# Optimization experiments

Measured on AMD Instinct MI355X. Metric: run time of the kernel, lower is better.

## Reference

```python
import jax, jax.numpy as jnp
import numpy as np

L, D, H, FF = 4, 256, 8, 1024
B, S = 4, 1024
HD = D // H
EPS = 1e-5


def layer_norm(x, g, b):
    mu = jnp.mean(x, axis=-1, keepdims=True)
    var = jnp.mean(jnp.square(x - mu), axis=-1, keepdims=True)
    return (x - mu) * jax.lax.rsqrt(var + EPS) * g + b


def setup_inputs() -> dict:
    key = jax.random.key(0)
    ks = jax.random.split(key, 16)
    sd = 0.02
    return {
        "x": jax.random.normal(ks[0], (B, S, D), dtype=jnp.float32),
        "mask": jnp.ones((B, S), dtype=jnp.int32),
        # per-layer stacked params (leading dim L); Linear stored as (in, out)
        "qkv_w": jax.random.normal(ks[1], (L, D, 3 * D), dtype=jnp.float32) * sd,
        "qkv_b": jnp.zeros((L, 3 * D), dtype=jnp.float32),
        "fc_w": jax.random.normal(ks[2], (L, D, D), dtype=jnp.float32) * sd,
        "fc_b": jnp.zeros((L, D), dtype=jnp.float32),
        "ln1_g": jnp.ones((L, D), dtype=jnp.float32),
        "ln1_b": jnp.zeros((L, D), dtype=jnp.float32),
        "ln2_g": jnp.ones((L, D), dtype=jnp.float32),
        "ln2_b": jnp.zeros((L, D), dtype=jnp.float32),
        "ff1_w": jax.random.normal(ks[3], (L, D, FF), dtype=jnp.float32) * sd,
        "ff1_b": jnp.zeros((L, FF), dtype=jnp.float32),
        "ff2_w": jax.random.normal(ks[4], (L, FF, D), dtype=jnp.float32) * sd,
        "ff2_b": jnp.zeros((L, D), dtype=jnp.float32),
    }


def reference(x, mask, qkv_w, qkv_b, fc_w, fc_b, ln1_g, ln1_b, ln2_g, ln2_b,
              ff1_w, ff1_b, ff2_w, ff2_b):
    # mask: 1 = valid token, 0 = pad
    neg_inf = jnp.finfo(x.dtype).min
    key_mask = (mask == 0)[:, None, None, :]  # [B,1,1,S]
    for l in range(L):
        residual = x
        qkv = x @ qkv_w[l] + qkv_b[l]                       # [B,S,3D]
        q, k, v = jnp.split(qkv, 3, axis=-1)
        q = q.reshape(B, S, H, HD).transpose(0, 2, 1, 3)    # [B,H,S,hd]
        k = k.reshape(B, S, H, HD).transpose(0, 2, 1, 3)
        v = v.reshape(B, S, H, HD).transpose(0, 2, 1, 3)
        attn = jnp.einsum('bhqd,bhkd->bhqk', q, k)          # scale=1 (scale=False)
        attn = jnp.where(key_mask, neg_inf, attn)
        attn = jax.nn.softmax(attn, axis=-1)
        o = jnp.einsum('bhqk,bhkd->bhqd', attn, v)
        o = o.transpose(0, 2, 1, 3).reshape(B, S, D)
        o = o @ fc_w[l] + fc_b[l]
        x = layer_norm(o + residual, ln1_g[l], ln1_b[l])    # after_norm=True
        residual = x
        h = jax.nn.relu(x @ ff1_w[l] + ff1_b[l])
        h = h @ ff2_w[l] + ff2_b[l]
        x = layer_norm(residual + h, ln2_g[l], ln2_b[l])
    return x
```

## Files before the change

### kernel.cpp

```cpp
#include <hip/hip_runtime.h>
#include <hip/hip_bf16.h>
#include <math.h>

#define NL 4
#define DMODEL 256
#define NH 8
#define FFDIM 1024
#define BB 4
#define SS 1024
#define HDIM 32
#define MROWS (BB * SS)
#define LN_EPS 1e-5f

typedef __bf16 bf16x8 __attribute__((ext_vector_type(8)));
typedef float f32x4 __attribute__((ext_vector_type(4)));
typedef short s16x4 __attribute__((ext_vector_type(4)));
typedef unsigned int u32;

__device__ __forceinline__ ushort f2bf(float f) {
    uint u = __builtin_bit_cast(uint, f);
    u += 0x7fff + ((u >> 16) & 1);
    return (ushort)(u >> 16);
}
__device__ __forceinline__ uint pack2(float a, float b) {
    return (uint)f2bf(a) | ((uint)f2bf(b) << 16);
}

__device__ __forceinline__ int xcd_swz(int bid, int nwg) {
    return (bid & 7) * (nwg >> 3) + (bid >> 3);
}

template<int N> __device__ __forceinline__ void vmcnt_wait() {
    asm volatile("s_waitcnt vmcnt(%0)" :: "n"(N) : "memory");
}
__device__ __forceinline__ void raw_barrier() {
    asm volatile("s_barrier" ::: "memory");
}
__device__ __forceinline__ void lgkm0() {
    asm volatile("s_waitcnt lgkmcnt(0)" ::: "memory");
}

__device__ __forceinline__ void async_ld16(const void* g, void* l) {
    __builtin_amdgcn_global_load_lds(
        (const __attribute__((address_space(1))) u32*)g,
        (__attribute__((address_space(3))) u32*)l, 16, 0, 0);
}

#if __has_builtin(__builtin_amdgcn_ds_read_tr16_b64)
#define TR_BUILTIN 1
#else
#define TR_BUILTIN 0
#endif

__device__ __forceinline__ s16x4 tr16(const ushort* p) {
    __attribute__((address_space(3))) s16x4* ap =
        (__attribute__((address_space(3))) s16x4*)p;
#if TR_BUILTIN
    return __builtin_amdgcn_ds_read_tr16_b64(ap);
#else
    s16x4 r;
    asm volatile("ds_read_b64_tr_b16 %0, %1" : "=v"(r) : "v"(ap) : "memory");
    return r;
#endif
}
__device__ __forceinline__ void tr_fence() {
#if !TR_BUILTIN
    asm volatile("s_waitcnt lgkmcnt(0)" ::: "memory");
    __builtin_amdgcn_sched_barrier(0);
#endif
}

__global__ __launch_bounds__(256)
void wconv_all(const float* __restrict__ qkv_w, const float* __restrict__ fc_w,
               const float* __restrict__ ff1_w, const float* __restrict__ ff2_w,
               ushort* __restrict__ wq, ushort* __restrict__ wfc,
               ushort* __restrict__ wf1, ushort* __restrict__ wf2)
{
    const int l = blockIdx.z;
    int t = blockIdx.x;
    const float* src; ushort* dst; int K, N, nx;
    if (t < 192)      {          src = qkv_w; dst = wq;  K = 256;  N = 768;  nx = 24; }
    else if (t < 256) { t -= 192; src = fc_w;  dst = wfc; K = 256;  N = 256;  nx = 8; }
    else if (t < 512) { t -= 256; src = ff1_w; dst = wf1; K = 256;  N = 1024; nx = 32; }
    else              { t -= 512; src = ff2_w; dst = wf2; K = 1024; N = 256;  nx = 8; }
    src += (size_t)l * K * N;
    dst += (size_t)l * K * N;
    const int n0 = (t % nx) * 32, k0 = (t / nx) * 32;

    __shared__ ushort tt[32][33];
    const int tn = threadIdx.x & 31, tk8 = threadIdx.x >> 5;
    #pragma unroll
    for (int i = 0; i < 4; ++i)
        tt[tn][tk8 + i * 8] = f2bf(src[(size_t)(k0 + tk8 + i * 8) * N + n0 + tn]);
    __syncthreads();
    #pragma unroll
    for (int i = 0; i < 4; ++i)
        dst[(size_t)(n0 + tk8 + i * 8) * K + k0 + tn] = tt[tk8 + i * 8][tn];
}

__global__ __launch_bounds__(256)
void convert_x(const float* __restrict__ xin, float* __restrict__ x,
               ushort* __restrict__ xb)
{
    const size_t i = ((size_t)blockIdx.x * 256 + threadIdx.x) * 4;
    const float4 v = *reinterpret_cast<const float4*>(xin + i);
    *reinterpret_cast<float4*>(x + i) = v;
    uint2 p = make_uint2(pack2(v.x, v.y), pack2(v.z, v.w));
    *reinterpret_cast<uint2*>(xb + i) = p;
}

template<int BM, int BN, int WM, int WN, int ACT, int OBF>
__global__ __launch_bounds__(256)
void gemm_mfma(const ushort* __restrict__ A, const ushort* __restrict__ WT,
               const float* __restrict__ bias, float* __restrict__ Cf,
               ushort* __restrict__ Cb, int N, int K)
{
    constexpr int BK = 64;
    constexpr int WR = BM / WM;
    constexpr int WC = BN / WN;
    constexpr int MR = WR / 16, NR = WC / 16;
    constexpr int LSTG = BM / 32 + BN / 32;
    __shared__ __align__(16) ushort As[2][BM * BK];
    __shared__ __align__(16) ushort Bs[2][BN * BK];

    const int tid = threadIdx.x;
    const int lin = blockIdx.y * gridDim.x + blockIdx.x;
    const int work = xcd_swz(lin, gridDim.x * gridDim.y);
    const int m0 = (work / gridDim.x) * BM, n0 = (work % gridDim.x) * BN;
    const int wid = tid >> 6, lane = tid & 63;
    const int g = lane >> 4, c = lane & 15;
    const int wr = wid / WN, wc = wid % WN;

    auto stage = [&](int buf, int k0) {
        #pragma unroll
        for (int it = 0; it < (BM * BK * 2) / 4096; ++it) {
            const int o = tid * 16 + it * 4096;
            const int r = o >> 7;
            const int cb = (o & 127) ^ ((r & 7) << 4);
            async_ld16(A + (size_t)(m0 + r) * K + k0 + (cb >> 1),
                       (char*)&As[buf][0] + o);
        }
        #pragma unroll
        for (int it = 0; it < (BN * BK * 2) / 4096; ++it) {
            const int o = tid * 16 + it * 4096;
            const int r = o >> 7;
            const int cb = (o & 127) ^ ((r & 7) << 4);
            async_ld16(WT + (size_t)(n0 + r) * K + k0 + (cb >> 1),
                       (char*)&Bs[buf][0] + o);
        }
    };

    f32x4 acc[MR][NR] = {};

    stage(0, 0);

    int cur = 0;
    for (int k0 = 0; k0 < K; k0 += BK, cur ^= 1) {
        if (k0 + BK < K) { stage(cur ^ 1, k0 + BK); vmcnt_wait<LSTG>(); }
        else             { vmcnt_wait<0>(); }
        raw_barrier();

        #pragma unroll
        for (int ks = 0; ks < 2; ++ks) {
            bf16x8 af[MR], bfr[NR];
            #pragma unroll
            for (int mi = 0; mi < MR; ++mi) {
                const int row = wr * WR + mi * 16 + c;
                af[mi] = *(const bf16x8*)((const char*)&As[cur][0]
                    + row * 128 + ((ks * 64 + g * 16) ^ ((row & 7) << 4)));
            }
            #pragma unroll
            for (int ni = 0; ni < NR; ++ni) {
                const int row = wc * WC + ni * 16 + c;
                bfr[ni] = *(const bf16x8*)((const char*)&Bs[cur][0]
                    + row * 128 + ((ks * 64 + g * 16) ^ ((row & 7) << 4)));
            }
            #pragma unroll
            for (int mi = 0; mi < MR; ++mi)
                #pragma unroll
                for (int ni = 0; ni < NR; ++ni)
                    acc[mi][ni] = __builtin_amdgcn_mfma_f32_16x16x32_bf16(
                        af[mi], bfr[ni], acc[mi][ni], 0, 0, 0);
        }
        raw_barrier();
    }

    float bv[NR];
    #pragma unroll
    for (int ni = 0; ni < NR; ++ni)
        bv[ni] = bias[n0 + wc * WC + ni * 16 + c];

    #pragma unroll
    for (int mi = 0; mi < MR; ++mi) {
        #pragma unroll
        for (int j = 0; j < 4; ++j) {
            const int row = m0 + wr * WR + mi * 16 + g * 4 + j;
            #pragma unroll
            for (int ni = 0; ni < NR; ++ni) {
                float v = acc[mi][ni][j] + bv[ni];
                if (ACT) v = fmaxf(v, 0.f);
                const int col = n0 + wc * WC + ni * 16 + c;
                if (OBF) Cb[(size_t)row * N + col] = f2bf(v);
                else     Cf[(size_t)row * N + col] = v;
            }
        }
    }
}

__global__ __launch_bounds__(512)
void mlp_fused(const ushort* __restrict__ Aattn, const ushort* __restrict__ Wfc,
               const float* __restrict__ bfc, const float* __restrict__ g1,
               const float* __restrict__ be1, const ushort* __restrict__ W1,
               const float* __restrict__ b1, const ushort* __restrict__ W2,
               const float* __restrict__ b2, const float* __restrict__ g2,
               const float* __restrict__ be2, float* __restrict__ x,
               ushort* __restrict__ xb)
{
    __shared__ __align__(16) ushort As3[3][16 * 64];
    __shared__ __align__(16) ushort Bs3[3][256 * 64];
    __shared__ __align__(16) ushort ybf[16 * 256];
    __shared__ __align__(16) ushort hbuf[16 * 1024];
    __shared__ float rsum[4][16], rsq[4][16], mval[16], ival[16];

    const int tid = threadIdx.x;
    const int m0 = blockIdx.x * 16;
    const int wid = tid >> 6, lane = tid & 63;
    const int g = lane >> 4, c = lane & 15;
    const bool consumer = (tid < 256);
    const int ptid = tid - 256;
    const int at = tid - 384;

    auto stage_step = [&](int s, int b) {
        const ushort* bsrc; int ldk;
        if (s < 4)       { bsrc = Wfc + s * 64; ldk = 256; }
        else if (s < 20) { const int t = s - 4;
                           bsrc = W1 + (size_t)((t >> 2) * 256) * 256 + (t & 3) * 64;
                           ldk = 256; }
        else             { const int t = s - 20; bsrc = W2 + t * 64; ldk = 1024; }
        #pragma unroll
        for (int it = 0; it < 8; ++it) {
            const int o = ptid * 16 + it * 4096;
            const int r = o >> 7;
            const int cb = (o & 127) ^ ((r & 7) << 4);
            async_ld16(bsrc + (size_t)r * ldk + (cb >> 1), (char*)&Bs3[b][0] + o);
        }
        if (s < 4 && at >= 0) {
            const int o = at * 16;
            const int r = o >> 7;
            const int cb = (o & 127) ^ ((r & 7) << 4);
            async_ld16(Aattn + (size_t)(m0 + r) * 256 + s * 64 + (cb >> 1),
                       (char*)&As3[b][0] + o);
        }
    };

    f32x4 acc[4] = {};
    float res[4][4];

    if (!consumer) {
        stage_step(0, 0);
        stage_step(1, 1);
        if (wid >= 6) vmcnt_wait<9>(); else vmcnt_wait<8>();
    }
    raw_barrier();

    #pragma unroll 1
    for (int s = 0; s < 36; ++s) {
        if (s == 4) {
            if (consumer) {
                float bv[4];
                #pragma unroll
                for (int ni = 0; ni < 4; ++ni)
                    bv[ni] = bfc[wid * 64 + ni * 16 + c];
                #pragma unroll
                for (int j = 0; j < 4; ++j) {
                    const int row = g * 4 + j;
                    float sm = 0.f;
                    #pragma unroll
                    for (int ni = 0; ni < 4; ++ni) {
                        const int col = wid * 64 + ni * 16 + c;
                        float vv = acc[ni][j] + bv[ni]
                                 + x[(size_t)(m0 + row) * 256 + col];
                        acc[ni][j] = vv;
                        sm += vv;
                    }
                    #pragma unroll
                    for (int off = 1; off < 16; off <<= 1) sm += __shfl_xor(sm, off);
                    if (c == 0) rsum[wid][row] = sm;
                }
            }
            lgkm0(); raw_barrier();
            if (consumer && tid < 16)
                mval[tid] = (rsum[0][tid] + rsum[1][tid] + rsum[2][tid]
                             + rsum[3][tid]) * (1.f / 256);
            lgkm0(); raw_barrier();
            if (consumer) {
                #pragma unroll
                for (int j = 0; j < 4; ++j) {
                    const int row = g * 4 + j;
                    const float mean = mval[row];
                    float q = 0.f;
                    #pragma unroll
                    for (int ni = 0; ni < 4; ++ni) {
                        const float d = acc[ni][j] - mean;
                        q += d * d;
                    }
                    #pragma unroll
                    for (int off = 1; off < 16; off <<= 1) q += __shfl_xor(q, off);
                    if (c == 0) rsq[wid][row] = q;
                }
            }
            lgkm0(); raw_barrier();
            if (consumer && tid < 16) {
                const float q = rsq[0][tid] + rsq[1][tid] + rsq[2][tid] + rsq[3][tid];
                ival[tid] = rsqrtf(q * (1.f / 256) + LN_EPS);
            }
            lgkm0(); raw_barrier();
            if (consumer) {
                float gl[4], bl[4];
                #pragma unroll
                for (int ni = 0; ni < 4; ++ni) {
                    const int col = wid * 64 + ni * 16 + c;
                    gl[ni] = g1[col]; bl[ni] = be1[col];
                }
                #pragma unroll
                for (int j = 0; j < 4; ++j) {
                    const int row = g * 4 + j;
                    const float mean = mval[row], inv = ival[row];
                    #pragma unroll
                    for (int ni = 0; ni < 4; ++ni) {
                        const int col = wid * 64 + ni * 16 + c;
                        const float y = (acc[ni][j] - mean) * inv * gl[ni] + bl[ni];
                        res[ni][j] = y;
                        const int byteo = row * 512 + ((col * 2) ^ ((row & 7) << 4));
                        *(ushort*)((char*)ybf + byteo) = f2bf(y);
                        acc[ni][j] = 0.f;
                    }
                }
            }
            lgkm0(); raw_barrier();
        }
        if (s == 20) { lgkm0(); raw_barrier(); }

        if (consumer) {
            const int b = s % 3;
            #pragma unroll
            for (int ks = 0; ks < 2; ++ks) {
                bf16x8 af;
                if (s < 4) {
                    af = *(const bf16x8*)((const char*)&As3[b][0]
                        + c * 128 + ((ks * 64 + g * 16) ^ ((c & 7) << 4)));
                } else if (s < 20) {
                    const int kk = (s - 4) & 3;
                    const int kbyte = (kk * 64 + ks * 32 + g * 8) * 2;
                    af = *(const bf16x8*)((const char*)ybf
                        + c * 512 + (kbyte ^ ((c & 7) << 4)));
                } else {
                    const int t = s - 20;
                    const int kbyte = (t * 64 + ks * 32 + g * 8) * 2;
                    af = *(const bf16x8*)((const char*)hbuf
                        + c * 2048 + (kbyte ^ ((c & 7) << 4)));
                }
                #pragma unroll
                for (int ni = 0; ni < 4; ++ni) {
                    const int row = wid * 64 + ni * 16 + c;
                    const bf16x8 bf = *(const bf16x8*)((const char*)&Bs3[b][0]
                        + row * 128 + ((ks * 64 + g * 16) ^ ((row & 7) << 4)));
                    acc[ni] = __builtin_amdgcn_mfma_f32_16x16x32_bf16(
                        af, bf, acc[ni], 0, 0, 0);
                }
            }
        } else {
            if (s + 2 < 36) {
                stage_step(s + 2, (s + 2) % 3);
                if (s + 2 < 4 && wid >= 6) vmcnt_wait<9>();
                else                       vmcnt_wait<8>();
            } else {
                vmcnt_wait<0>();
            }
        }
        raw_barrier();

        if (consumer && s >= 4 && s < 20 && ((s - 4) & 3) == 3) {
            const int nt = (s - 4) >> 2;
            #pragma unroll
            for (int j = 0; j < 4; ++j) {
                const int row = g * 4 + j;
                #pragma unroll
                for (int ni = 0; ni < 4; ++ni) {
                    const int col = nt * 256 + wid * 64 + ni * 16 + c;
                    const float h = fmaxf(acc[ni][j] + b1[col], 0.f);
                    const int byteo = row * 2048 + ((col * 2) ^ ((row & 7) << 4));
                    *(ushort*)((char*)hbuf + byteo) = f2bf(h);
                    acc[ni][j] = 0.f;
                }
            }
        }
    }

    if (consumer) {
        float bv[4];
        #pragma unroll
        for (int ni = 0; ni < 4; ++ni)
            bv[ni] = b2[wid * 64 + ni * 16 + c];
        #pragma unroll
        for (int j = 0; j < 4; ++j) {
            const int row = g * 4 + j;
            float sm = 0.f;
            #pragma unroll
            for (int ni = 0; ni < 4; ++ni) {
                float vv = acc[ni][j] + bv[ni] + res[ni][j];
                acc[ni][j] = vv;
                sm += vv;
            }
            #pragma unroll
            for (int off = 1; off < 16; off <<= 1) sm += __shfl_xor(sm, off);
            if (c == 0) rsum[wid][row] = sm;
        }
    }
    lgkm0(); raw_barrier();
    if (consumer && tid < 16)
        mval[tid] = (rsum[0][tid] + rsum[1][tid] + rsum[2][tid] + rsum[3][tid])
                    * (1.f / 256);
    lgkm0(); raw_barrier();
    if (consumer) {
        #pragma unroll
        for (int j = 0; j < 4; ++j) {
            const int row = g * 4 + j;
            const float mean = mval[row];
            float q = 0.f;
            #pragma unroll
            for (int ni = 0; ni < 4; ++ni) {
                const float d = acc[ni][j] - mean;
                q += d * d;
            }
            #pragma unroll
            for (int off = 1; off < 16; off <<= 1) q += __shfl_xor(q, off);
            if (c == 0) rsq[wid][row] = q;
        }
    }
    lgkm0(); raw_barrier();
    if (consumer && tid < 16) {
        const float q = rsq[0][tid] + rsq[1][tid] + rsq[2][tid] + rsq[3][tid];
        ival[tid] = rsqrtf(q * (1.f / 256) + LN_EPS);
    }
    lgkm0(); raw_barrier();
    if (consumer) {
        float gl[4], bl[4];
        #pragma unroll
        for (int ni = 0; ni < 4; ++ni) {
            const int col = wid * 64 + ni * 16 + c;
            gl[ni] = g2[col]; bl[ni] = be2[col];
        }
        #pragma unroll
        for (int j = 0; j < 4; ++j) {
            const int row = g * 4 + j;
            const float mean = mval[row], inv = ival[row];
            #pragma unroll
            for (int ni = 0; ni < 4; ++ni) {
                const int col = wid * 64 + ni * 16 + c;
                const float y = (acc[ni][j] - mean) * inv * gl[ni] + bl[ni];
                x[(size_t)(m0 + row) * 256 + col] = y;
                xb[(size_t)(m0 + row) * 256 + col] = f2bf(y);
            }
        }
    }
}

__global__ __launch_bounds__(512)
void attn_mfma8(const ushort* __restrict__ qkv, const int* __restrict__ mask,
                ushort* __restrict__ out)
{
    const int tid = threadIdx.x;
    const int lane = tid & 63, wid = tid >> 6;
    const int g = lane >> 4, c = lane & 15;
    const int work = xcd_swz(blockIdx.x, 256);
    const int qblk = work & 7;
    const int bh = work >> 3;
    const int h = bh & (NH - 1), b = bh >> 3;
    const int q0 = qblk * 128 + wid * 16;

    __shared__ __align__(16) ushort Kb[2][128 * 32];
    __shared__ __align__(16) ushort Vs[2][2][128][16];
    __shared__ __align__(16) ushort Pl[8][16][136];
    __shared__ __align__(16) float  sbias[SS];
    __shared__ int mflag[8];

    const ushort* base  = qkv + (size_t)b * SS * 768;
    const ushort* kbase = base + DMODEL + h * HDIM;
    const ushort* vbase = base + 2 * DMODEL + h * HDIM;

    {
        const int i = tid * 2;
        const int2 mv = *reinterpret_cast<const int2*>(mask + b * SS + i);
        float2 bv;
        bv.x = mv.x ? 0.f : -3.4e38f;
        bv.y = mv.y ? 0.f : -3.4e38f;
        *reinterpret_cast<float2*>(&sbias[i]) = bv;
        const int miss = __any(!(mv.x && mv.y));
        if (lane == 0) mflag[wid] = miss;
    }

    const bf16x8 qfrag = *(const bf16x8*)(
        base + (size_t)(q0 + c) * 768 + h * HDIM + g * 8);

    const int o16   = tid * 16;
    const int krow  = o16 >> 6;
    const int kin   = (o16 & 63) ^ ((krow & 3) << 4);
    const int vhalf = o16 >> 12;
    const int vkey  = (o16 & 4095) >> 5;
    const int vd    = vhalf * 16 + (((o16 >> 4) & 1) << 3);

    #define STAGE(buf, koff)                                                   \
        do {                                                                   \
            async_ld16(kbase + (size_t)((koff) + krow) * 768 + (kin >> 1),     \
                       (char*)&Kb[buf][0] + o16);                              \
            async_ld16(vbase + (size_t)((koff) + vkey) * 768 + vd,             \
                       (char*)&Vs[buf][0][0][0] + o16);                        \
        } while (0)

    STAGE(0, 0);
    lgkm0();
    raw_barrier();
    const int anyMasked = mflag[0] | mflag[1] | mflag[2] | mflag[3]
                        | mflag[4] | mflag[5] | mflag[6] | mflag[7];

    float m = -1e30f, lpart = 0.f;
    f32x4 o0 = {0.f, 0.f, 0.f, 0.f}, o1 = {0.f, 0.f, 0.f, 0.f};
    const f32x4 zf = {0.f, 0.f, 0.f, 0.f};

    for (int t = 0; t < 8; ++t) {
        const int cur = t & 1;
        if (t < 7) { STAGE(cur ^ 1, (t + 1) * 128); vmcnt_wait<2>(); }
        else       { vmcnt_wait<0>(); }
        raw_barrier();

        f32x4 s[8];
        __builtin_amdgcn_s_setprio(1);
        #pragma unroll
        for (int kt = 0; kt < 8; ++kt) {
            const int row = kt * 16 + c;
            const bf16x8 kf = *(const bf16x8*)((const char*)&Kb[cur][0]
                + row * 64 + ((g * 16) ^ ((c & 3) << 4)));
            s[kt] = __builtin_amdgcn_mfma_f32_16x16x32_bf16(kf, qfrag, zf, 0, 0, 0);
        }
        __builtin_amdgcn_s_setprio(0);

        if (anyMasked) {
            #pragma unroll
            for (int kt = 0; kt < 8; ++kt) {
                const f32x4 bv = *reinterpret_cast<const f32x4*>(
                    &sbias[t * 128 + kt * 16 + g * 4]);
                #pragma unroll
                for (int r = 0; r < 4; ++r) s[kt][r] += bv[r];
            }
        }

        union UU { s16x4 h[2]; bf16x8 v; };
        UU u0[4], u1[4];
        #pragma unroll
        for (int ks = 0; ks < 4; ++ks) {
            const int vr0 = ks * 32 + g * 8;
            u0[ks].h[0] = tr16(&Vs[cur][0][vr0][c]);
            u0[ks].h[1] = tr16(&Vs[cur][0][vr0 + 4][c]);
            u1[ks].h[0] = tr16(&Vs[cur][1][vr0][c]);
            u1[ks].h[1] = tr16(&Vs[cur][1][vr0 + 4][c]);
        }

        float mx = fmaxf(fmaxf(s[0][0], s[0][1]), fmaxf(s[0][2], s[0][3]));
        #pragma unroll
        for (int kt = 1; kt < 8; ++kt)
            mx = fmaxf(mx, fmaxf(fmaxf(s[kt][0], s[kt][1]),
                                 fmaxf(s[kt][2], s[kt][3])));
        if (!__all(mx <= m + 8.f)) {
            float fm = fmaxf(mx, __shfl_xor(mx, 16));
            fm = fmaxf(fm, __shfl_xor(fm, 32));
            const float mn = fmaxf(m, fm);
            const float sc = __expf(m - mn);
            m = mn;
            lpart *= sc;
            float scr[4];
            #pragma unroll
            for (int r = 0; r < 4; ++r) scr[r] = __shfl(sc, g * 4 + r);
            #pragma unroll
            for (int r = 0; r < 4; ++r) { o0[r] *= scr[r]; o1[r] *= scr[r]; }
        }

        float ls = 0.f;
        #pragma unroll
        for (int kt = 0; kt < 8; ++kt) {
            const float p0 = __expf(s[kt][0] - m);
            const float p1 = __expf(s[kt][1] - m);
            const float p2 = __expf(s[kt][2] - m);
            const float p3 = __expf(s[kt][3] - m);
            ls += (p0 + p1) + (p2 + p3);
            uint2 pk2 = make_uint2(pack2(p0, p1), pack2(p2, p3));
            *reinterpret_cast<uint2*>(&Pl[wid][c][kt * 16 + g * 4]) = pk2;
        }
        lpart += ls;

        tr_fence();
        __builtin_amdgcn_s_setprio(1);
        #pragma unroll
        for (int ks = 0; ks < 4; ++ks) {
            const bf16x8 pa = *(const bf16x8*)&Pl[wid][c][ks * 32 + g * 8];
            o0 = __builtin_amdgcn_mfma_f32_16x16x32_bf16(pa, u0[ks].v, o0, 0, 0, 0);
            o1 = __builtin_amdgcn_mfma_f32_16x16x32_bf16(pa, u1[ks].v, o1, 0, 0, 0);
        }
        __builtin_amdgcn_s_setprio(0);
        raw_barrier();
    }
    #undef STAGE

    float lsum = lpart;
    lsum += __shfl_xor(lsum, 16);
    lsum += __shfl_xor(lsum, 32);
    const float rs = 1.f / lsum;
    float inv[4];
    #pragma unroll
    for (int r = 0; r < 4; ++r) inv[r] = __shfl(rs, g * 4 + r);
    #pragma unroll
    for (int r = 0; r < 4; ++r) {
        ushort* op = out + (size_t)(b * SS + q0 + g * 4 + r) * DMODEL + h * HDIM;
        op[c]      = f2bf(o0[r] * inv[r]);
        op[16 + c] = f2bf(o1[r] * inv[r]);
    }
}

extern "C" void kernel_launch(void* const* d_in, const int* in_sizes, int n_in,
                              void* d_out, int out_size, void* d_ws, size_t ws_size,
                              hipStream_t stream)
{
    const float* x_in   = (const float*)d_in[0];
    const int*   maskp  = (const int*)d_in[1];
    const float* qkv_w  = (const float*)d_in[2];
    const float* qkv_b  = (const float*)d_in[3];
    const float* fc_w   = (const float*)d_in[4];
    const float* fc_b   = (const float*)d_in[5];
    const float* ln1_g  = (const float*)d_in[6];
    const float* ln1_b  = (const float*)d_in[7];
    const float* ln2_g  = (const float*)d_in[8];
    const float* ln2_b  = (const float*)d_in[9];
    const float* ff1_w  = (const float*)d_in[10];
    const float* ff1_b  = (const float*)d_in[11];
    const float* ff2_w  = (const float*)d_in[12];
    const float* ff2_b  = (const float*)d_in[13];

    float* x = (float*)d_out;

    ushort* wt_qkv = (ushort*)d_ws;
    ushort* wt_fc  = wt_qkv + (size_t)NL * 768 * 256;
    ushort* wt_ff1 = wt_fc  + (size_t)NL * 256 * 256;
    ushort* wt_ff2 = wt_ff1 + (size_t)NL * 1024 * 256;
    ushort* big    = wt_ff2 + (size_t)NL * 256 * 1024;
    ushort* attn_bf= big + (size_t)MROWS * FFDIM;
    ushort* x_bf   = attn_bf + (size_t)MROWS * DMODEL;

    wconv_all<<<dim3(768, 1, NL), 256, 0, stream>>>(
        qkv_w, fc_w, ff1_w, ff2_w, wt_qkv, wt_fc, wt_ff1, wt_ff2);
    convert_x<<<dim3(MROWS * DMODEL / 1024), 256, 0, stream>>>(x_in, x, x_bf);

    for (int l = 0; l < NL; ++l) {
        gemm_mfma<64, 64, 2, 2, 0, 1><<<dim3(12, 64), 256, 0, stream>>>(
            x_bf, wt_qkv + (size_t)l * 768 * 256, qkv_b + l * 768,
            nullptr, big, 768, 256);
        attn_mfma8<<<dim3(256), 512, 0, stream>>>(big, maskp, attn_bf);
        mlp_fused<<<dim3(256), 512, 0, stream>>>(
            attn_bf, wt_fc + (size_t)l * 256 * 256, fc_b + l * 256,
            ln1_g + l * DMODEL, ln1_b + l * DMODEL,
            wt_ff1 + (size_t)l * 1024 * 256, ff1_b + l * FFDIM,
            wt_ff2 + (size_t)l * 256 * 1024, ff2_b + l * DMODEL,
            ln2_g + l * DMODEL, ln2_b + l * DMODEL, x, x_bf);
    }
}
```

Before: 230.2 us.

## Replace producer/consumer warp split in fused MLP with all-warp compute and loads

```diff
diff --git a/kernel.cpp b/kernel.cpp
--- a/kernel.cpp
+++ b/kernel.cpp
@@ -220,17 +220,15 @@
     __shared__ __align__(16) ushort Bs3[3][256 * 64];
     __shared__ __align__(16) ushort ybf[16 * 256];
     __shared__ __align__(16) ushort hbuf[16 * 1024];
-    __shared__ float rsum[4][16], rsq[4][16], mval[16], ival[16];
+    __shared__ float rsum[8][16], rsq[8][16], mval[16], ival[16];
 
     const int tid = threadIdx.x;
     const int m0 = blockIdx.x * 16;
     const int wid = tid >> 6, lane = tid & 63;
     const int g = lane >> 4, c = lane & 15;
-    const bool consumer = (tid < 256);
-    const int ptid = tid - 256;
-    const int at = tid - 384;
-
-    auto stage_step = [&](int s, int b) {
+
+    auto stage_step = [&](int s) {
+        const int b = s % 3;
         const ushort* bsrc; int ldk;
         if (s < 4)       { bsrc = Wfc + s * 64; ldk = 256; }
         else if (s < 20) { const int t = s - 4;
@@ -238,14 +236,14 @@
                            ldk = 256; }
         else             { const int t = s - 20; bsrc = W2 + t * 64; ldk = 1024; }
         #pragma unroll
-        for (int it = 0; it < 8; ++it) {
-            const int o = ptid * 16 + it * 4096;
+        for (int it = 0; it < 4; ++it) {
+            const int o = tid * 16 + it * 8192;
             const int r = o >> 7;
             const int cb = (o & 127) ^ ((r & 7) << 4);
             async_ld16(bsrc + (size_t)r * ldk + (cb >> 1), (char*)&Bs3[b][0] + o);
         }
-        if (s < 4 && at >= 0) {
-            const int o = at * 16;
+        if (s < 4 && tid < 128) {
+            const int o = tid * 16;
             const int r = o >> 7;
             const int cb = (o & 127) ^ ((r & 7) << 4);
             async_ld16(Aattn + (size_t)(m0 + r) * 256 + s * 64 + (cb >> 1),
@@ -253,141 +251,126 @@
         }
     };
 
-    f32x4 acc[4] = {};
-    float res[4][4];
-
-    if (!consumer) {
-        stage_step(0, 0);
-        stage_step(1, 1);
-        if (wid >= 6) vmcnt_wait<9>(); else vmcnt_wait<8>();
-    }
-    raw_barrier();
+    f32x4 acc[2] = {};
+    float res[2][4];
+
+    stage_step(0);
+    stage_step(1);
 
     #pragma unroll 1
     for (int s = 0; s < 36; ++s) {
         if (s == 4) {
-            if (consumer) {
-                float bv[4];
-                #pragma unroll
-                for (int ni = 0; ni < 4; ++ni)
-                    bv[ni] = bfc[wid * 64 + ni * 16 + c];
-                #pragma unroll
-                for (int j = 0; j < 4; ++j) {
-                    const int row = g * 4 + j;
-                    float sm = 0.f;
-                    #pragma unroll
-                    for (int ni = 0; ni < 4; ++ni) {
-                        const int col = wid * 64 + ni * 16 + c;
-                        float vv = acc[ni][j] + bv[ni]
-                                 + x[(size_t)(m0 + row) * 256 + col];
-                        acc[ni][j] = vv;
-                        sm += vv;
-                    }
-                    #pragma unroll
-                    for (int off = 1; off < 16; off <<= 1) sm += __shfl_xor(sm, off);
-                    if (c == 0) rsum[wid][row] = sm;
-                }
-            }
-            lgkm0(); raw_barrier();
-            if (consumer && tid < 16)
-                mval[tid] = (rsum[0][tid] + rsum[1][tid] + rsum[2][tid]
-                             + rsum[3][tid]) * (1.f / 256);
-            lgkm0(); raw_barrier();
-            if (consumer) {
-                #pragma unroll
-                for (int j = 0; j < 4; ++j) {
-                    const int row = g * 4 + j;
-                    const float mean = mval[row];
-                    float q = 0.f;
-                    #pragma unroll
-                    for (int ni = 0; ni < 4; ++ni) {
-                        const float d = acc[ni][j] - mean;
-                        q += d * d;
-                    }
-                    #pragma unroll
-                    for (int off = 1; off < 16; off <<= 1) q += __shfl_xor(q, off);
-                    if (c == 0) rsq[wid][row] = q;
-                }
-            }
-            lgkm0(); raw_barrier();
-            if (consumer && tid < 16) {
-                const float q = rsq[0][tid] + rsq[1][tid] + rsq[2][tid] + rsq[3][tid];
-                ival[tid] = rsqrtf(q * (1.f / 256) + LN_EPS);
-            }
-            lgkm0(); raw_barrier();
-            if (consumer) {
-                float gl[4], bl[4];
-                #pragma unroll
-                for (int ni = 0; ni < 4; ++ni) {
-                    const int col = wid * 64 + ni * 16 + c;
-                    gl[ni] = g1[col]; bl[ni] = be1[col];
-                }
-                #pragma unroll
-                for (int j = 0; j < 4; ++j) {
-                    const int row = g * 4 + j;
-                    const float mean = mval[row], inv = ival[row];
-                    #pragma unroll
-                    for (int ni = 0; ni < 4; ++ni) {
-                        const int col = wid * 64 + ni * 16 + c;
-                        const float y = (acc[ni][j] - mean) * inv * gl[ni] + bl[ni];
-                        res[ni][j] = y;
-                        const int byteo = row * 512 + ((col * 2) ^ ((row & 7) << 4));
-                        *(ushort*)((char*)ybf + byteo) = f2bf(y);
-                        acc[ni][j] = 0.f;
-                    }
-                }
-            }
-            lgkm0(); raw_barrier();
-        }
-        if (s == 20) { lgkm0(); raw_barrier(); }
-
-        if (consumer) {
-            const int b = s % 3;
-            #pragma unroll
-            for (int ks = 0; ks < 2; ++ks) {
-                bf16x8 af;
-                if (s < 4) {
-                    af = *(const bf16x8*)((const char*)&As3[b][0]
-                        + c * 128 + ((ks * 64 + g * 16) ^ ((c & 7) << 4)));
-                } else if (s < 20) {
-                    const int kk = (s - 4) & 3;
-                    const int kbyte = (kk * 64 + ks * 32 + g * 8) * 2;
-                    af = *(const bf16x8*)((const char*)ybf
-                        + c * 512 + (kbyte ^ ((c & 7) << 4)));
-                } else {
-                    const int t = s - 20;
-                    const int kbyte = (t * 64 + ks * 32 + g * 8) * 2;
-                    af = *(const bf16x8*)((const char*)hbuf
-                        + c * 2048 + (kbyte ^ ((c & 7) << 4)));
-                }
-                #pragma unroll
-                for (int ni = 0; ni < 4; ++ni) {
-                    const int row = wid * 64 + ni * 16 + c;
-                    const bf16x8 bf = *(const bf16x8*)((const char*)&Bs3[b][0]
-                        + row * 128 + ((ks * 64 + g * 16) ^ ((row & 7) << 4)));
-                    acc[ni] = __builtin_amdgcn_mfma_f32_16x16x32_bf16(
-                        af, bf, acc[ni], 0, 0, 0);
-                }
-            }
-        } else {
-            if (s + 2 < 36) {
-                stage_step(s + 2, (s + 2) % 3);
-                if (s + 2 < 4 && wid >= 6) vmcnt_wait<9>();
-                else                       vmcnt_wait<8>();
-            } else {
-                vmcnt_wait<0>();
-            }
-        }
-        raw_barrier();
-
-        if (consumer && s >= 4 && s < 20 && ((s - 4) & 3) == 3) {
-            const int nt = (s - 4) >> 2;
+            float bv[2], gl[2], bl[2];
+            #pragma unroll
+            for (int ni = 0; ni < 2; ++ni) {
+                const int col = wid * 32 + ni * 16 + c;
+                bv[ni] = bfc[col]; gl[ni] = g1[col]; bl[ni] = be1[col];
+            }
             #pragma unroll
             for (int j = 0; j < 4; ++j) {
                 const int row = g * 4 + j;
-                #pragma unroll
-                for (int ni = 0; ni < 4; ++ni) {
-                    const int col = nt * 256 + wid * 64 + ni * 16 + c;
+                float sm = 0.f;
+                #pragma unroll
+                for (int ni = 0; ni < 2; ++ni) {
+                    const int col = wid * 32 + ni * 16 + c;
+                    float vv = acc[ni][j] + bv[ni] + x[(size_t)(m0 + row) * 256 + col];
+                    acc[ni][j] = vv;
+                    sm += vv;
+                }
+                #pragma unroll
+                for (int off = 1; off < 16; off <<= 1) sm += __shfl_xor(sm, off);
+                if (c == 0) rsum[wid][row] = sm;
+            }
+            lgkm0(); raw_barrier();
+            if (tid < 16)
+                mval[tid] = (rsum[0][tid] + rsum[1][tid] + rsum[2][tid] + rsum[3][tid]
+                           + rsum[4][tid] + rsum[5][tid] + rsum[6][tid] + rsum[7][tid])
+                            * (1.f / 256);
+            lgkm0(); raw_barrier();
+            #pragma unroll
+            for (int j = 0; j < 4; ++j) {
+                const int row = g * 4 + j;
+                const float mean = mval[row];
+                float q = 0.f;
+                #pragma unroll
+                for (int ni = 0; ni < 2; ++ni) {
+                    const float d = acc[ni][j] - mean;
+                    q += d * d;
+                }
+                #pragma unroll
+                for (int off = 1; off < 16; off <<= 1) q += __shfl_xor(q, off);
+                if (c == 0) rsq[wid][row] = q;
+            }
+            lgkm0(); raw_barrier();
+            if (tid < 16) {
+                const float q = rsq[0][tid] + rsq[1][tid] + rsq[2][tid] + rsq[3][tid]
+                              + rsq[4][tid] + rsq[5][tid] + rsq[6][tid] + rsq[7][tid];
+                ival[tid] = rsqrtf(q * (1.f / 256) + LN_EPS);
+            }
+            lgkm0(); raw_barrier();
+            #pragma unroll
+            for (int j = 0; j < 4; ++j) {
+                const int row = g * 4 + j;
+                const float mean = mval[row], inv = ival[row];
+                #pragma unroll
+                for (int ni = 0; ni < 2; ++ni) {
+                    const int col = wid * 32 + ni * 16 + c;
+                    const float y = (acc[ni][j] - mean) * inv * gl[ni] + bl[ni];
+                    res[ni][j] = y;
+                    const int byteo = row * 512 + ((col * 2) ^ ((row & 7) << 4));
+                    *(ushort*)((char*)ybf + byteo) = f2bf(y);
+                    acc[ni][j] = 0.f;
+                }
+            }
+            lgkm0(); raw_barrier();
+        }
+        if (s == 20) { lgkm0(); raw_barrier(); }
+
+        if (s < 35) {
+            if (s + 1 < 4) { if (tid < 128) vmcnt_wait<5>(); else vmcnt_wait<4>(); }
+            else           { vmcnt_wait<4>(); }
+        } else {
+            vmcnt_wait<0>();
+        }
+        raw_barrier();
+        if (s + 2 < 36) stage_step(s + 2);
+
+        const int b = s % 3;
+        #pragma unroll
+        for (int ks = 0; ks < 2; ++ks) {
+            bf16x8 af;
+            if (s < 4) {
+                af = *(const bf16x8*)((const char*)&As3[b][0]
+                    + c * 128 + ((ks * 64 + g * 16) ^ ((c & 7) << 4)));
+            } else if (s < 20) {
+                const int kk = (s - 4) & 3;
+                const int kbyte = (kk * 64 + ks * 32 + g * 8) * 2;
+                af = *(const bf16x8*)((const char*)ybf
+                    + c * 512 + (kbyte ^ ((c & 7) << 4)));
+            } else {
+                const int t = s - 20;
+                const int kbyte = (t * 64 + ks * 32 + g * 8) * 2;
+                af = *(const bf16x8*)((const char*)hbuf
+                    + c * 2048 + (kbyte ^ ((c & 7) << 4)));
+            }
+            #pragma unroll
+            for (int ni = 0; ni < 2; ++ni) {
+                const int row = wid * 32 + ni * 16 + c;
+                const bf16x8 bf = *(const bf16x8*)((const char*)&Bs3[b][0]
+                    + row * 128 + ((ks * 64 + g * 16) ^ ((row & 7) << 4)));
+                acc[ni] = __builtin_amdgcn_mfma_f32_16x16x32_bf16(
+                    af, bf, acc[ni], 0, 0, 0);
+            }
+        }
+
+        if (s >= 4 && s < 20 && ((s - 4) & 3) == 3) {
+            const int nt = (s - 4) >> 2;
+            #pragma unroll
+            for (int j = 0; j < 4; ++j) {
+                const int row = g * 4 + j;
+                #pragma unroll
+                for (int ni = 0; ni < 2; ++ni) {
+                    const int col = nt * 256 + wid * 32 + ni * 16 + c;
                     const float h = fmaxf(acc[ni][j] + b1[col], 0.f);
                     const int byteo = row * 2048 + ((col * 2) ^ ((row & 7) << 4));
                     *(ushort*)((char*)hbuf + byteo) = f2bf(h);
@@ -397,17 +380,19 @@
         }
     }
 
-    if (consumer) {
-        float bv[4];
-        #pragma unroll
-        for (int ni = 0; ni < 4; ++ni)
-            bv[ni] = b2[wid * 64 + ni * 16 + c];
+    {
+        float bv[2], gl[2], bl[2];
+        #pragma unroll
+        for (int ni = 0; ni < 2; ++ni) {
+            const int col = wid * 32 + ni * 16 + c;
+            bv[ni] = b2[col]; gl[ni] = g2[col]; bl[ni] = be2[col];
+        }
         #pragma unroll
         for (int j = 0; j < 4; ++j) {
             const int row = g * 4 + j;
             float sm = 0.f;
             #pragma unroll
-            for (int ni = 0; ni < 4; ++ni) {
+            for (int ni = 0; ni < 2; ++ni) {
                 float vv = acc[ni][j] + bv[ni] + res[ni][j];
                 acc[ni][j] = vv;
                 sm += vv;
@@ -416,20 +401,19 @@
             for (int off = 1; off < 16; off <<= 1) sm += __shfl_xor(sm, off);
             if (c == 0) rsum[wid][row] = sm;
         }
-    }
-    lgkm0(); raw_barrier();
-    if (consumer && tid < 16)
-        mval[tid] = (rsum[0][tid] + rsum[1][tid] + rsum[2][tid] + rsum[3][tid])
-                    * (1.f / 256);
-    lgkm0(); raw_barrier();
-    if (consumer) {
+        lgkm0(); raw_barrier();
+        if (tid < 16)
+            mval[tid] = (rsum[0][tid] + rsum[1][tid] + rsum[2][tid] + rsum[3][tid]
+                       + rsum[4][tid] + rsum[5][tid] + rsum[6][tid] + rsum[7][tid])
+                        * (1.f / 256);
+        lgkm0(); raw_barrier();
         #pragma unroll
         for (int j = 0; j < 4; ++j) {
             const int row = g * 4 + j;
             const float mean = mval[row];
             float q = 0.f;
             #pragma unroll
-            for (int ni = 0; ni < 4; ++ni) {
+            for (int ni = 0; ni < 2; ++ni) {
                 const float d = acc[ni][j] - mean;
                 q += d * d;
             }
@@ -437,27 +421,20 @@
             for (int off = 1; off < 16; off <<= 1) q += __shfl_xor(q, off);
             if (c == 0) rsq[wid][row] = q;
         }
-    }
-    lgkm0(); raw_barrier();
-    if (consumer && tid < 16) {
-        const float q = rsq[0][tid] + rsq[1][tid] + rsq[2][tid] + rsq[3][tid];
-        ival[tid] = rsqrtf(q * (1.f / 256) + LN_EPS);
-    }
-    lgkm0(); raw_barrier();
-    if (consumer) {
-        float gl[4], bl[4];
-        #pragma unroll
-        for (int ni = 0; ni < 4; ++ni) {
-            const int col = wid * 64 + ni * 16 + c;
-            gl[ni] = g2[col]; bl[ni] = be2[col];
-        }
+        lgkm0(); raw_barrier();
+        if (tid < 16) {
+            const float q = rsq[0][tid] + rsq[1][tid] + rsq[2][tid] + rsq[3][tid]
+                          + rsq[4][tid] + rsq[5][tid] + rsq[6][tid] + rsq[7][tid];
+            ival[tid] = rsqrtf(q * (1.f / 256) + LN_EPS);
+        }
+        lgkm0(); raw_barrier();
         #pragma unroll
         for (int j = 0; j < 4; ++j) {
             const int row = g * 4 + j;
             const float mean = mval[row], inv = ival[row];
             #pragma unroll
-            for (int ni = 0; ni < 4; ++ni) {
-                const int col = wid * 64 + ni * 16 + c;
+            for (int ni = 0; ni < 2; ++ni) {
+                const int col = wid * 32 + ni * 16 + c;
                 const float y = (acc[ni][j] - mean) * inv * gl[ni] + bl[ni];
                 x[(size_t)(m0 + row) * 256 + col] = y;
                 xb[(size_t)(m0 + row) * 256 + col] = f2bf(y);
```

After: 281.0 us. 22.1% more time.
